# Kernel optimization log

Measured on AMD Instinct MI355X. Metric: run time of the kernel, lower is better.

## Reference

```python
import jax, jax.numpy as jnp
import numpy as np
from jax import lax

B, C, H, W = 256, 10, 256, 256


def _dilate4(m):
    # 4-connected dilation of a boolean mask [B, H, W]
    up = jnp.pad(m[:, 1:, :], ((0, 0), (0, 1), (0, 0)))
    down = jnp.pad(m[:, :-1, :], ((0, 0), (1, 0), (0, 0)))
    left = jnp.pad(m[:, :, 1:], ((0, 0), (0, 0), (0, 1)))
    right = jnp.pad(m[:, :, :-1], ((0, 0), (0, 0), (1, 0)))
    return up | down | left | right


def setup_inputs() -> dict:
    key = jax.random.key(0)
    grid = jax.random.uniform(key, (B, C, H, W), dtype=jnp.float32)
    return {"grid": grid, "seed_y": 100, "seed_x": 100, "target_color": 3}


def reference(grid, seed_y, seed_x, target_color):
    Bs, Cs, Hs, Ws = grid.shape
    # seed color: first channel c with grid[b, c, y, x] > 0.5 (argmax gives first True)
    present = grid[:, :, seed_y, seed_x] > 0.5          # [B, C]
    has_seed = jnp.any(present, axis=1)                  # [B]
    seed_color = jnp.argmax(present, axis=1)             # [B]
    # occupancy mask of the seed-color channel, per batch element
    color_mask = (
        jnp.take_along_axis(grid, seed_color[:, None, None, None], axis=1)[:, 0] > 0.5
    )                                                    # [B, H, W]
    # BFS == iterative label propagation to a fixed point
    init = jnp.zeros((Bs, Hs, Ws), dtype=bool).at[:, seed_y, seed_x].set(has_seed)

    def cond(state):
        return state[1]

    def body(state):
        m, _ = state
        nm = (m | _dilate4(m)) & color_mask
        return nm, jnp.any(nm != m)

    mask, _ = lax.while_loop(cond, body, (init, jnp.array(True)))

    # result[b, seed_color][mask] = 0 ; then result[b, target_color][mask] = 1
    cid = jnp.arange(Cs)[None, :, None, None]            # [1, C, 1, 1]
    sc = seed_color[:, None, None, None]                 # [B, 1, 1, 1]
    m4 = mask[:, None, :, :]                             # [B, 1, H, W]
    out = jnp.where(m4 & (cid == sc), jnp.float32(0), grid)
    out = jnp.where(m4 & (cid == target_color), jnp.float32(1), out)
    return out
```

## Files before the change

kernel.cpp:

```cpp
#include <hip/hip_runtime.h>
#include <stdint.h>

#define B_ 256
#define C_ 10
#define H_ 256
#define W_ 256
#define WPR 8
#define WPI 2048

typedef float f4 __attribute__((ext_vector_type(4)));

__device__ __forceinline__ uint32_t spread4(uint32_t u) {
  u = (u | (u << 12)) & 0x000F000Fu;
  u = (u | (u << 6))  & 0x03030303u;
  u = (u | (u << 3))  & 0x11111111u;
  return u;
}

__global__ __launch_bounds__(256) void ff_seed_kernel(
    const float* __restrict__ grid,
    const int* __restrict__ p_sy, const int* __restrict__ p_sx,
    int* __restrict__ ws_sc, int* __restrict__ ws_has)
{
  const int b = blockIdx.x * 256 + threadIdx.x;
  if (b >= B_) return;
  const int sy = p_sy[0], sx = p_sx[0];
  int sc = 0, has = 0;
  #pragma unroll
  for (int c = C_ - 1; c >= 0; --c) {
    float v = grid[(((size_t)b * C_ + c) * H_ + sy) * W_ + sx];
    if (v > 0.5f) { sc = c; has = 1; }
  }
  ws_sc[b] = sc;
  ws_has[b] = has;
}

__global__ __launch_bounds__(256) void ff_bitmask_kernel(
    const float* __restrict__ grid,
    const int* __restrict__ ws_sc,
    uint32_t* __restrict__ ws_cm)
{
  const int lane = threadIdx.x & 63;
  const int wv   = threadIdx.x >> 6;
  int gw = blockIdx.x * 4 + wv;
  const int nw = gridDim.x * 4;
  const int nchunks = B_ * H_ * W_ / 256;
  for (int ck = gw; ck < nchunks; ck += nw) {
    const int b   = ck >> 8;
    const int cof = ck & 255;
    const int sc  = ws_sc[b];
    const float* ch = grid + ((size_t)b * C_ + sc) * (size_t)(H_ * W_) + cof * 256;
    f4 v = ((const f4*)ch)[lane];
    unsigned long long bx = __ballot(v.x > 0.5f);
    unsigned long long by = __ballot(v.y > 0.5f);
    unsigned long long bz = __ballot(v.z > 0.5f);
    unsigned long long bw = __ballot(v.w > 0.5f);
    if (lane < 8) {
      uint32_t word = spread4((uint32_t)(bx >> (8 * lane)) & 0xFFu)
                    | (spread4((uint32_t)(by >> (8 * lane)) & 0xFFu) << 1)
                    | (spread4((uint32_t)(bz >> (8 * lane)) & 0xFFu) << 2)
                    | (spread4((uint32_t)(bw >> (8 * lane)) & 0xFFu) << 3);
      ws_cm[(size_t)b * WPI + cof * 8 + lane] = word;
    }
  }
}

__global__ __launch_bounds__(256) void ff_flood_kernel(
    const uint32_t* __restrict__ ws_cm,
    const int* __restrict__ ws_has,
    const int* __restrict__ p_sy, const int* __restrict__ p_sx,
    uint32_t* __restrict__ ws_mask)
{
  const int b = blockIdx.x, tid = threadIdx.x;
  const int lane = tid & 63;
  const int r = tid;
  __shared__ uint32_t cm[WPI];
  __shared__ uint32_t m[WPI];
  __shared__ int s_changed;

  const int sy = p_sy[0], sx = p_sx[0];

  for (int i = tid; i < WPI; i += 256) {
    cm[(i & 7) * H_ + (i >> 3)] = ws_cm[(size_t)b * WPI + i];
    m[(i & 7) * H_ + (i >> 3)] = 0u;
  }
  if (tid == 0) {
    s_changed = 0;
    if (ws_has[b]) m[(sx >> 5) * H_ + sy] = 1u << (sx & 31);
  }
  __syncthreads();

  uint32_t cmr[WPR];
  #pragma unroll
  for (int j = 0; j < WPR; ++j) cmr[j] = cm[j * H_ + r];

  for (;;) {
    uint32_t w_[WPR], orig[WPR], abv[WPR], blw[WPR];
    #pragma unroll
    for (int j = 0; j < WPR; ++j) {
      w_[j] = m[j * H_ + r];
      orig[j] = w_[j];
      abv[j] = (lane == 0 && r > 0)        ? m[j * H_ + (r - 1)] : 0u;
      blw[j] = (lane == 63 && r < H_ - 1)  ? m[j * H_ + (r + 1)] : 0u;
    }

    for (;;) {
      bool hch = true;
      while (hch) {
        hch = false;
        #pragma unroll
        for (int j = 0; j < WPR; ++j) {
          uint32_t lo = (w_[j] << 1) | (j > 0       ? (w_[j - 1] >> 31) : 0u);
          uint32_t hi = (w_[j] >> 1) | (j < WPR - 1 ? (w_[j + 1] << 31) : 0u);
          uint32_t v = (w_[j] | lo | hi) & cmr[j];
          hch |= (v != w_[j]);
          w_[j] = v;
        }
        hch = __any(hch);
      }
      bool vch = false;
      #pragma unroll
      for (int j = 0; j < WPR; ++j) {
        uint32_t up = __shfl_up(w_[j], 1);
        if (lane == 0) up = abv[j];
        uint32_t dn = __shfl_down(w_[j], 1);
        if (lane == 63) dn = blw[j];
        uint32_t v = (w_[j] | up | dn) & cmr[j];
        vch |= (v != w_[j]);
        w_[j] = v;
      }
      if (!__any(vch)) break;
    }

    bool ch = false;
    #pragma unroll
    for (int j = 0; j < WPR; ++j) ch |= (w_[j] != orig[j]);
    if (ch) {
      #pragma unroll
      for (int j = 0; j < WPR; ++j) m[j * H_ + r] = w_[j];
      s_changed = 1;
    }
    __syncthreads();
    bool done = (s_changed == 0);
    __syncthreads();
    if (done) break;
    if (tid == 0) s_changed = 0;
    __syncthreads();
  }

  for (int i = tid; i < WPI; i += 256)
    ws_mask[(size_t)b * WPI + i] = m[(i & 7) * H_ + (i >> 3)];
}

__global__ __launch_bounds__(256) void ff_copy_kernel(
    const f4* __restrict__ gin, f4* __restrict__ gout)
{
  const int i = blockIdx.x * 256 + threadIdx.x;
  f4 v = __builtin_nontemporal_load(&gin[i]);
  __builtin_nontemporal_store(v, &gout[i]);
}

__global__ __launch_bounds__(256) void ff_fixup_kernel(
    float* __restrict__ out,
    const uint32_t* __restrict__ ws_mask,
    const int* __restrict__ ws_sc,
    const int* __restrict__ p_tc)
{
  const int b = blockIdx.x, tid = threadIdx.x;
  const int tc = p_tc[0];
  const int sc = ws_sc[b];
  float* osc = out + ((size_t)b * C_ + sc) * (size_t)(H_ * W_);
  float* otc = out + ((size_t)b * C_ + tc) * (size_t)(H_ * W_);
  const bool same = (sc == tc);
  #pragma unroll
  for (int k = 0; k < WPI / 256; ++k) {
    const int i = k * 256 + tid;
    uint32_t mw = ws_mask[(size_t)b * WPI + i];
    while (mw) {
      const int bit = __ffs(mw) - 1;
      mw &= mw - 1;
      const int pix = (i << 5) | bit;
      if (!same) osc[pix] = 0.0f;
      otc[pix] = 1.0f;
    }
  }
}

extern "C" void kernel_launch(void* const* d_in, const int* in_sizes, int n_in,
                              void* d_out, int out_size, void* d_ws, size_t ws_size,
                              hipStream_t stream) {
  const float* grid = (const float*)d_in[0];
  const int* p_sy   = (const int*)d_in[1];
  const int* p_sx   = (const int*)d_in[2];
  const int* p_tc   = (const int*)d_in[3];
  float* out        = (float*)d_out;

  uint32_t* ws_mask = (uint32_t*)d_ws;
  uint32_t* ws_cm   = (uint32_t*)((char*)d_ws + 2u * 1024 * 1024);
  int* ws_sc        = (int*)((char*)d_ws + 4u * 1024 * 1024);
  int* ws_has       = (int*)((char*)d_ws + 4u * 1024 * 1024 + 4096);

  ff_seed_kernel<<<1, 256, 0, stream>>>(grid, p_sy, p_sx, ws_sc, ws_has);
  ff_bitmask_kernel<<<2048, 256, 0, stream>>>(grid, ws_sc, ws_cm);
  ff_flood_kernel<<<B_, 256, 0, stream>>>(ws_cm, ws_has, p_sy, p_sx, ws_mask);

  const int n4 = (B_ * C_ * H_ * W_) / 4;
  ff_copy_kernel<<<n4 / 256, 256, 0, stream>>>((const f4*)grid, (f4*)out);
  ff_fixup_kernel<<<B_, 256, 0, stream>>>(out, ws_mask, ws_sc, p_tc);
}
```

Before: 288.5 us.

## Fuse bitmask build into grid copy and scatter fixup inside flood kernel

The color-mask bitmask is now computed inside the full grid copy kernel, so the seed-color channel is read once instead of twice. The fixup writes now happen directly from the flood kernel's register-held final mask, which drops the mask round-trip through workspace and two kernel launches. The trade-off is a divergent ballot branch added to the bandwidth-bound copy. The scatter writes now come from only 256 blocks rather than running after a separate copy pass.

```diff
diff --git a/kernel.cpp b/kernel.cpp
--- a/kernel.cpp
+++ b/kernel.cpp
@@ -7,6 +7,7 @@
 #define W_ 256
 #define WPR 8
 #define WPI 2048
+#define N4  (B_ * C_ * H_ * W_ / 4)
 
 typedef float f4 __attribute__((ext_vector_type(4)));
 
@@ -35,22 +36,21 @@
   ws_has[b] = has;
 }
 
-__global__ __launch_bounds__(256) void ff_bitmask_kernel(
-    const float* __restrict__ grid,
+__global__ __launch_bounds__(256) void ff_copy_bitmask_kernel(
+    const f4* __restrict__ gin, f4* __restrict__ gout,
     const int* __restrict__ ws_sc,
     uint32_t* __restrict__ ws_cm)
 {
-  const int lane = threadIdx.x & 63;
-  const int wv   = threadIdx.x >> 6;
-  int gw = blockIdx.x * 4 + wv;
-  const int nw = gridDim.x * 4;
-  const int nchunks = B_ * H_ * W_ / 256;
-  for (int ck = gw; ck < nchunks; ck += nw) {
-    const int b   = ck >> 8;
-    const int cof = ck & 255;
-    const int sc  = ws_sc[b];
-    const float* ch = grid + ((size_t)b * C_ + sc) * (size_t)(H_ * W_) + cof * 256;
-    f4 v = ((const f4*)ch)[lane];
+  const int i = blockIdx.x * 256 + threadIdx.x;
+  f4 v = __builtin_nontemporal_load(&gin[i]);
+  __builtin_nontemporal_store(v, &gout[i]);
+
+  const int bc = blockIdx.x >> 6;
+  const int b  = bc / C_;
+  const int c  = bc - b * C_;
+  if (c == ws_sc[b]) {
+    const int lane = threadIdx.x & 63;
+    const int wv   = threadIdx.x >> 6;
     unsigned long long bx = __ballot(v.x > 0.5f);
     unsigned long long by = __ballot(v.y > 0.5f);
     unsigned long long bz = __ballot(v.z > 0.5f);
@@ -60,16 +60,19 @@
                     | (spread4((uint32_t)(by >> (8 * lane)) & 0xFFu) << 1)
                     | (spread4((uint32_t)(bz >> (8 * lane)) & 0xFFu) << 2)
                     | (spread4((uint32_t)(bw >> (8 * lane)) & 0xFFu) << 3);
-      ws_cm[(size_t)b * WPI + cof * 8 + lane] = word;
+      const int wbase = ((blockIdx.x & 63) << 5) + (wv << 3);
+      ws_cm[(size_t)b * WPI + wbase + lane] = word;
     }
   }
 }
 
-__global__ __launch_bounds__(256) void ff_flood_kernel(
+__global__ __launch_bounds__(256) void ff_flood_scatter_kernel(
     const uint32_t* __restrict__ ws_cm,
+    const int* __restrict__ ws_sc,
     const int* __restrict__ ws_has,
     const int* __restrict__ p_sy, const int* __restrict__ p_sx,
-    uint32_t* __restrict__ ws_mask)
+    const int* __restrict__ p_tc,
+    float* __restrict__ out)
 {
   const int b = blockIdx.x, tid = threadIdx.x;
   const int lane = tid & 63;
@@ -94,8 +97,9 @@
   #pragma unroll
   for (int j = 0; j < WPR; ++j) cmr[j] = cm[j * H_ + r];
 
+  uint32_t w_[WPR];
   for (;;) {
-    uint32_t w_[WPR], orig[WPR], abv[WPR], blw[WPR];
+    uint32_t orig[WPR], abv[WPR], blw[WPR];
     #pragma unroll
     for (int j = 0; j < WPR; ++j) {
       w_[j] = m[j * H_ + r];
@@ -148,38 +152,18 @@
     __syncthreads();
   }
 
-  for (int i = tid; i < WPI; i += 256)
-    ws_mask[(size_t)b * WPI + i] = m[(i & 7) * H_ + (i >> 3)];
-}
-
-__global__ __launch_bounds__(256) void ff_copy_kernel(
-    const f4* __restrict__ gin, f4* __restrict__ gout)
-{
-  const int i = blockIdx.x * 256 + threadIdx.x;
-  f4 v = __builtin_nontemporal_load(&gin[i]);
-  __builtin_nontemporal_store(v, &gout[i]);
-}
-
-__global__ __launch_bounds__(256) void ff_fixup_kernel(
-    float* __restrict__ out,
-    const uint32_t* __restrict__ ws_mask,
-    const int* __restrict__ ws_sc,
-    const int* __restrict__ p_tc)
-{
-  const int b = blockIdx.x, tid = threadIdx.x;
   const int tc = p_tc[0];
   const int sc = ws_sc[b];
+  const bool same = (sc == tc);
   float* osc = out + ((size_t)b * C_ + sc) * (size_t)(H_ * W_);
   float* otc = out + ((size_t)b * C_ + tc) * (size_t)(H_ * W_);
-  const bool same = (sc == tc);
   #pragma unroll
-  for (int k = 0; k < WPI / 256; ++k) {
-    const int i = k * 256 + tid;
-    uint32_t mw = ws_mask[(size_t)b * WPI + i];
+  for (int j = 0; j < WPR; ++j) {
+    uint32_t mw = w_[j];
     while (mw) {
       const int bit = __ffs(mw) - 1;
       mw &= mw - 1;
-      const int pix = (i << 5) | bit;
+      const int pix = r * W_ + (j << 5) + bit;
       if (!same) osc[pix] = 0.0f;
       otc[pix] = 1.0f;
     }
@@ -195,16 +179,13 @@
   const int* p_tc   = (const int*)d_in[3];
   float* out        = (float*)d_out;
 
-  uint32_t* ws_mask = (uint32_t*)d_ws;
-  uint32_t* ws_cm   = (uint32_t*)((char*)d_ws + 2u * 1024 * 1024);
-  int* ws_sc        = (int*)((char*)d_ws + 4u * 1024 * 1024);
-  int* ws_has       = (int*)((char*)d_ws + 4u * 1024 * 1024 + 4096);
+  uint32_t* ws_cm   = (uint32_t*)d_ws;
+  int* ws_sc        = (int*)((char*)d_ws + 2u * 1024 * 1024);
+  int* ws_has       = (int*)((char*)d_ws + 2u * 1024 * 1024 + 4096);
 
   ff_seed_kernel<<<1, 256, 0, stream>>>(grid, p_sy, p_sx, ws_sc, ws_has);
-  ff_bitmask_kernel<<<2048, 256, 0, stream>>>(grid, ws_sc, ws_cm);
-  ff_flood_kernel<<<B_, 256, 0, stream>>>(ws_cm, ws_has, p_sy, p_sx, ws_mask);
-
-  const int n4 = (B_ * C_ * H_ * W_) / 4;
-  ff_copy_kernel<<<n4 / 256, 256, 0, stream>>>((const f4*)grid, (f4*)out);
-  ff_fixup_kernel<<<B_, 256, 0, stream>>>(out, ws_mask, ws_sc, p_tc);
+  ff_copy_bitmask_kernel<<<N4 / 256, 256, 0, stream>>>(
+      (const f4*)grid, (f4*)out, ws_sc, ws_cm);
+  ff_flood_scatter_kernel<<<B_, 256, 0, stream>>>(
+      ws_cm, ws_sc, ws_has, p_sy, p_sx, p_tc, out);
 }
```

After: 274.5 us, median of 2. 1.05x faster.
